# Performance work log

Measured on AMD Instinct MI355X. Metric: run time of the kernel, lower is better.

Reference implementation:

```python
import jax, jax.numpy as jnp
import numpy as np

BITWIDTH = 8
T = 1 << BITWIDTH          # bit-stream length = 2**bitwidth = 256
B = 16                     # independent unary streams
IN1, H1, H2, OUT = 1024, 512, 256, 10


def sobol_rng(bitwidth=BITWIDTH):
    # 1-D unscrambled Sobol sequence (== torch.quasirandom.SobolEngine(1)),
    n = 1 << bitwidth
    i = np.arange(n, dtype=np.uint32)
    g = i ^ (i >> 1)  # Gray code
    x = np.zeros(n, dtype=np.float64)
    for j in range(bitwidth):
        x += ((g >> np.uint32(j)) & np.uint32(1)).astype(np.float64) * 2.0 ** -(j + 1)
    return jnp.asarray(x * 2.0 - 1.0, dtype=jnp.float32)


def _forward(w1, b1, w2, b2, w3, b3, prediction, x):
    rng = sobol_rng()
    f32 = jnp.float32
    Bn = x.shape[1]

    def lin_state(fin, fout):
        # rng_wght_idx rows are all identical in the torch code (the [1, fin]
        # input broadcasts across [fout, fin]), so we keep only [B, fin].
        return (jnp.zeros((Bn, fin), jnp.int32),   # rng_wght_idx
                jnp.zeros((Bn, fin), jnp.int32),   # rng_wght_idx_inv
                jnp.zeros((Bn, fout), f32),        # in_accumulator
                jnp.zeros((Bn, fout), f32))        # out_accumulator

    def ulinear(state, xf, xi, w, bvec, t, offset):
        cum, cum_inv, in_acc, out_acc = state
        # regenerate binary weight matrices by compare against gathered rng
        w_pos = (w[None, :, :] > rng[cum][:, None, :]).astype(f32)      # [B, fout, fin]
        w_neg = (w[None, :, :] <= rng[cum_inv][:, None, :]).astype(f32)  # [B, fout, fin]
        bias_bit = (bvec > rng[t]).astype(f32)                           # [fout]
        y = (jnp.einsum('bi,boi->bo', xf, w_pos)
             + jnp.einsum('bi,boi->bo', 1.0 - xf, w_neg)
             + bias_bit[None, :])
        in_acc = in_acc + y - offset
        out = (in_acc > out_acc).astype(f32)
        out_acc = out_acc + out
        return (cum + xi, cum_inv + (1 - xi), in_acc, out_acc), out

    def ucompare(acc, inp):  # unary ReLU (UnaryCompare)
        sign = (acc < 0).astype(f32)
        out = sign + (1.0 - sign) * inp
        return acc + 2.0 * out - 1.0, out

    def step(carry, xs_t):
        s1, c1, s2, c2, s3 = carry
        xi, t = xs_t
        xf = xi.astype(f32)
        s1, y1 = ulinear(s1, xf, xi, w1, b1, t, (IN1 - 1) / 2)
        c1, a1 = ucompare(c1, y1)
        s2, y2 = ulinear(s2, a1, a1.astype(jnp.int32), w2, b2, t, (H1 - 1) / 2)
        c2, a2 = ucompare(c2, y2)
        s3, y3 = ulinear(s3, a2, a2.astype(jnp.int32), w3, b3, t, (H2 - 1) / 2)
        # ProgressivePrecision is re-created every forward: out_pp = 2*y3 - 1,
        # err = out_pp - prediction, then log_softmax.
        out_t = jax.nn.log_softmax(2.0 * y3 - 1.0 - prediction, axis=1)
        return (s1, c1, s2, c2, s3), out_t

    init = (lin_state(IN1, H1), jnp.zeros((Bn, H1), f32),
            lin_state(H1, H2), jnp.zeros((Bn, H2), f32),
            lin_state(H2, OUT))
    _, outs = jax.lax.scan(step, init, (x, jnp.arange(T)))
    return outs  # [T, B, OUT]


def setup_inputs():
    key = jax.random.key(0)
    ks = jax.random.split(key, 8)
    u = lambda k, s: jax.random.uniform(k, s, jnp.float32, -1.0, 1.0)
    return {
        'w1': u(ks[0], (H1, IN1)), 'b1': u(ks[1], (H1,)),
        'w2': u(ks[2], (H2, H1)), 'b2': u(ks[3], (H2,)),
        'w3': u(ks[4], (OUT, H2)), 'b3': u(ks[5], (OUT,)),
        'prediction': 0.1 * jax.random.normal(ks[6], (B, OUT), jnp.float32),
        'x': jax.random.randint(ks[7], (T, B, IN1), 0, 2, jnp.int32),
    }


def reference(w1, b1, w2, b2, w3, b3, prediction, x):
    return _forward(w1, b1, w2, b2, w3, b3, prediction, x)
```

## Files before the change

### kernel.cpp

```cpp
#include <hip/hip_runtime.h>
#include <stdint.h>

#define TSTEPS 256
#define NB 16
#define NM (TSTEPS*NB)

typedef short s16x2 __attribute__((ext_vector_type(2)));

__device__ __forceinline__ uint32_t perm8(int i) {
  uint32_t g = (uint32_t)(i ^ (i >> 1));
  return __brev(g) >> 24;
}

__device__ __forceinline__ void qstep3s(uint32_t& acc, uint32_t t2, uint32_t a2,
                                        uint32_t e2, uint32_t c15) {
  uint32_t z, z2;
  asm("v_pk_mad_i16 %0, %1, %2, %3" : "=v"(z) : "v"(a2), "s"(t2), "v"(e2));
  asm("v_pk_ashrrev_i16 %0, %1, %2" : "=v"(z2) : "v"(c15), "v"(z));
  asm("v_pk_add_i16 %0, %0, %1" : "+v"(acc) : "v"(z2));
}

__device__ __forceinline__ void qstep3(uint32_t& acc, uint32_t t2, uint32_t a2,
                                       uint32_t e2, uint32_t c15) {
  uint32_t z;
  asm("v_pk_mad_i16 %0, %2, %3, %4\n\t"
      "v_pk_ashrrev_i16 %0, %5, %0\n\t"
      "v_pk_add_i16 %1, %1, %0"
      : "=&v"(z), "+v"(acc)
      : "v"(a2), "v"(t2), "v"(e2), "v"(c15));
}

__device__ __forceinline__ uint32_t pkadd16(uint32_t a, uint32_t b) {
  return __builtin_bit_cast(uint32_t,
        (s16x2)(__builtin_bit_cast(s16x2, a) + __builtin_bit_cast(s16x2, b)));
}

__device__ __forceinline__ void unpackAE(uint32_t v2, uint32_t& a2, uint32_t& e2) {
  s16x2 sv = __builtin_bit_cast(s16x2, v2) >> 15;
  uint32_t su = __builtin_bit_cast(uint32_t, sv);
  uint32_t vand = v2 & 0x01FF01FFu;
  e2 = pkadd16(~vand, su & 0x01FF01FFu);
  a2 = pkadd16(0x00010001u, pkadd16(su, su));
}

__device__ __forceinline__ int rank256(float w) {
  double v = 128.0 * (double)w + 128.0;
  int t = (int)ceil(v);
  if (t < 0) t = 0; if (t > 256) t = 256;
  return t;
}

__global__ __launch_bounds__(256) void k_prepA(
    const float* __restrict__ w1, const float* __restrict__ w2,
    const float* __restrict__ w3, const float* __restrict__ b1,
    const float* __restrict__ b2, const float* __restrict__ b3,
    const int* __restrict__ x,
    uint32_t* __restrict__ T1, uint32_t* __restrict__ T2,
    uint32_t* __restrict__ T3t, uint32_t* __restrict__ bb1,
    uint32_t* __restrict__ bb2, uint32_t* __restrict__ bb3,
    uint16_t* __restrict__ cs)
{
  int bid = blockIdx.x, tid = threadIdx.x;
  if (bid < 1024) {
    int e = bid * 256 + tid;
    T1[e] = (uint32_t)rank256(w1[2 * e]) |
            ((uint32_t)rank256(w1[2 * e + 1]) << 16);
  } else if (bid < 1280) {
    int e = (bid - 1024) * 256 + tid;
    T2[e] = (uint32_t)rank256(w2[2 * e]) |
            ((uint32_t)rank256(w2[2 * e + 1]) << 16);
  } else if (bid < 1285) {
    int e = (bid - 1280) * 256 + tid;
    if (e < 1280) {
      int n = e % 10, kp = e / 10;
      T3t[e] = (uint32_t)rank256(w3[n * 256 + 2 * kp]) |
               ((uint32_t)rank256(w3[n * 256 + 2 * kp + 1]) << 16);
    }
  } else if (bid < 1301) {
    int w = (bid - 1285) * 256 + tid;
    int o = w >> 3, j = w & 7;
    double bv = (double)b1[o] * 128.0 + 128.0;
    uint32_t bits = 0;
    for (int s = 0; s < 32; ++s)
      if (bv > (double)perm8(j * 32 + s)) bits |= 1u << s;
    bb1[w] = bits;
  } else if (bid < 1309) {
    int w = (bid - 1301) * 256 + tid;
    int o = w >> 3, j = w & 7;
    double bv = (double)b2[o] * 128.0 + 128.0;
    uint32_t bits = 0;
    for (int s = 0; s < 32; ++s)
      if (bv > (double)perm8(j * 32 + s)) bits |= 1u << s;
    bb2[w] = bits;
  } else if (bid == 1309) {
    if (tid < 80) {
      int o = tid >> 3, j = tid & 7;
      double bv = (double)b3[o] * 128.0 + 128.0;
      uint32_t bits = 0;
      for (int s = 0; s < 32; ++s)
        if (bv > (double)perm8(j * 32 + s)) bits |= 1u << s;
      bb3[tid] = bits;
    }
  } else {
    int g = (bid - 1310) * 256 + tid;
    int i = g & 1023, b = (g >> 10) & 15, c = g >> 14;
    int s = 0, t0 = c * 32;
    for (int tt = t0; tt < t0 + 32; ++tt)
      s += x[((size_t)tt * NB + b) * 1024 + i];
    cs[(c * NB + b) * 1024 + i] = (uint16_t)s;
  }
}

__global__ __launch_bounds__(256) void k_prep1(const int* __restrict__ x,
                                               const uint16_t* __restrict__ cs,
                                               uint16_t* __restrict__ V1) {
  int g = blockIdx.x * 256 + threadIdx.x;
  int i = g & 1023, b = (g >> 10) & 15, c = g >> 14;
  int cum = 0;
  for (int cc = 0; cc < c; ++cc) cum += cs[(cc * NB + b) * 1024 + i];
  int t0 = c * 32;
  for (int tt = t0; tt < t0 + 32; ++tt) {
    int m = b * 256 + tt;
    int xv = x[((size_t)tt * NB + b) * 1024 + i];
    int idx = xv ? cum : (tt - cum);
    uint32_t p = perm8(idx);
    V1[(size_t)m * 1024 + i] =
        (uint16_t)((xv ? p : (510u - p)) | ((uint32_t)(xv ^ 1) << 15));
    cum += xv;
  }
}

template<int KD, int NT, int NREG, int KC>
__global__ __launch_bounds__(256, 4) void k_gemmv4(
    const uint16_t* __restrict__ V, const uint32_t* __restrict__ T,
    uint8_t* __restrict__ Yp)
{
  const int tid = threadIdx.x;
  const int m = blockIdx.x * 256 + tid;
  const int n0 = blockIdx.y * NREG;
  const int sk = blockIdx.z;
  const int k0 = sk * KC;
  const uint32_t c15 = 0x000F000Fu;
  uint32_t acc[NREG];
  #pragma unroll
  for (int nn = 0; nn < NREG; ++nn) acc[nn] = 0;
  const uint4* vsrc = (const uint4*)(V + (size_t)m * KD + k0);
  const uint32_t* tbase = T + (size_t)n0 * (KD / 2) + (k0 >> 1);
  #pragma unroll 1
  for (int c = 0; c < KC / 8; ++c) {
    uint4 vv = vsrc[c];
    uint32_t a0, e0, a1, e1, a2v, e2v, a3, e3;
    unpackAE(vv.x, a0, e0);
    unpackAE(vv.y, a1, e1);
    unpackAE(vv.z, a2v, e2v);
    unpackAE(vv.w, a3, e3);
    asm volatile("" : "+v"(a0), "+v"(e0), "+v"(a1), "+v"(e1),
                      "+v"(a2v), "+v"(e2v), "+v"(a3), "+v"(e3));
    #pragma unroll
    for (int nn = 0; nn < NREG; ++nn) {
      uint4 tw = *(const uint4*)(tbase + (size_t)nn * (KD / 2) + c * 4);
      qstep3s(acc[nn], tw.x, a0, e0, c15);
      qstep3s(acc[nn], tw.y, a1, e1, c15);
      qstep3s(acc[nn], tw.z, a2v, e2v, c15);
      qstep3s(acc[nn], tw.w, a3, e3, c15);
    }
  }
  uint8_t* outp = Yp + ((size_t)sk * NT + n0) * (size_t)NM + m;
  #pragma unroll
  for (int nn = 0; nn < NREG; ++nn) {
    uint32_t s = acc[nn];
    int cnt = KC + (int)(short)(s & 0xFFFFu) + (int)(short)(s >> 16);
    outp[(size_t)nn * NM] = (uint8_t)cnt;
  }
}

__global__ __launch_bounds__(256) void k_sumY(
    const uint8_t* __restrict__ Yp, uint16_t* __restrict__ Ys,
    int nwords, size_t plane_words, int SK)
{
  int i = blockIdx.x * 256 + threadIdx.x;
  if (i >= nwords) return;
  const uint32_t* p = (const uint32_t*)Yp;
  uint32_t aL = 0, aH = 0;
  for (int s = 0; s < SK; ++s) {
    uint32_t w = p[(size_t)s * plane_words + i];
    aL = pkadd16(aL, w & 0x00FF00FFu);
    aH = pkadd16(aH, (w >> 8) & 0x00FF00FFu);
  }
  uint2 o;
  o.x = (aL & 0xFFFFu) | (aH << 16);
  o.y = (aL >> 16) | (aH & 0xFFFF0000u);
  ((uint2*)Ys)[i] = o;
}

template<int NOUT, int OFF2, int LOGN>
__global__ __launch_bounds__(64) void k_scanv2(
    const uint16_t* __restrict__ Ys, const uint32_t* __restrict__ bb,
    uint16_t* __restrict__ Vn)
{
  int g = blockIdx.x * 64 + threadIdx.x;
  int o = g & (NOUT - 1);
  int b = g >> LOGN;
  const uint16_t* row = Ys + (size_t)o * NM + b * 256;
  int in2 = 0, out2 = 0, c2 = 0, cum = 0;
  uint4 cur = *(const uint4*)row;
  #pragma unroll
  for (int w = 0; w < 8; ++w) {
    uint32_t bwc = bb[o * 8 + w];
    #pragma unroll
    for (int cchunk = 0; cchunk < 4; ++cchunk) {
      int t0 = w * 32 + cchunk * 8;
      uint4 nxt = cur;
      if (t0 < 248) nxt = *(const uint4*)(row + t0 + 8);
      uint32_t cw[4] = {cur.x, cur.y, cur.z, cur.w};
      #pragma unroll
      for (int j = 0; j < 8; ++j) {
        int t = t0 + j;
        int cnt = (int)((cw[j >> 1] >> ((j & 1) * 16)) & 0xFFFFu);
        int bit = (int)((bwc >> (t & 31)) & 1u);
        in2 += 2 * cnt + 2 * bit - OFF2;
        int outb = (in2 > out2) ? 1 : 0;
        out2 += outb << 1;
        int a = (c2 < 0) ? 1 : outb;
        c2 += (a << 2) - 2;
        int idx = a ? cum : (t - cum);
        cum += a;
        uint32_t p = perm8(idx);
        Vn[(size_t)(b * 256 + t) * NOUT + o] =
            (uint16_t)((a ? p : (510u - p)) | ((uint32_t)(a ^ 1) << 15));
      }
      cur = nxt;
    }
  }
}

__global__ __launch_bounds__(256) void k_l3(
    const uint16_t* __restrict__ V3, const uint32_t* __restrict__ T3t,
    uint16_t* __restrict__ y3)
{
  __shared__ uint32_t T3s[128][16];
  __shared__ uint32_t UFs3[16][258];
  int tid = threadIdx.x;
  int m0 = blockIdx.x * 16;
  const uint32_t c15 = 0x000F000Fu;
  for (int j = tid; j < 2048; j += 256) {
    int kp = j >> 4, o2 = j & 15;
    T3s[kp][o2] = (o2 < 10) ? T3t[kp * 10 + o2] : 0u;
  }
  { int row = tid >> 4, part = tid & 15;
    const uint4* src = (const uint4*)(V3 + (size_t)(m0 + row) * 256 + part * 16);
    uint4 pa = src[0], pb = src[1];
    uint32_t w[8] = {pa.x, pa.y, pa.z, pa.w, pb.x, pb.y, pb.z, pb.w};
    uint32_t o[16];
    #pragma unroll
    for (int q = 0; q < 8; ++q) unpackAE(w[q], o[q * 2], o[q * 2 + 1]);
    #pragma unroll
    for (int q4 = 0; q4 < 4; ++q4)
      *(uint4*)&UFs3[row][part * 16 + q4 * 4] =
          make_uint4(o[q4 * 4], o[q4 * 4 + 1], o[q4 * 4 + 2], o[q4 * 4 + 3]);
  }
  __syncthreads();
  int mr = tid >> 4, o = tid & 15;
  uint32_t acc = 0;
  #pragma unroll 4
  for (int kp2 = 0; kp2 < 64; ++kp2) {
    uint4 uf = *(const uint4*)&UFs3[mr][kp2 * 4];
    qstep3(acc, T3s[2 * kp2][o],     uf.x, uf.y, c15);
    qstep3(acc, T3s[2 * kp2 + 1][o], uf.z, uf.w, c15);
  }
  if (o < 10)
    y3[(size_t)(m0 + mr) * 16 + o] =
        (uint16_t)(256 + (short)(acc & 0xFFFFu) + (short)(acc >> 16));
}

__global__ __launch_bounds__(256) void k_scan3sm(
    const uint16_t* __restrict__ y3, const uint32_t* __restrict__ bb3,
    const float* __restrict__ pred, float* __restrict__ out)
{
  __shared__ uint32_t obl[16][16][8];
  __shared__ float prs[160];
  int tid = threadIdx.x;
  if (tid < 160) prs[tid] = pred[tid];
  int b = tid >> 4, o = tid & 15;
  if (o < 10) {
    const uint16_t* row = y3 + (size_t)b * 256 * 16 + o;
    int in2 = 0, out2 = 0;
    #pragma unroll
    for (int w = 0; w < 8; ++w) {
      uint32_t bwc = bb3[o * 8 + w];
      uint32_t bits = 0;
      for (int s = 0; s < 32; ++s) {
        int cnt = row[(w * 32 + s) * 16];
        in2 += 2 * cnt + 2 * (int)((bwc >> s) & 1u) - 255;
        int outb = (in2 > out2) ? 1 : 0;
        out2 += outb << 1;
        bits |= (uint32_t)outb << s;
      }
      obl[b][o][w] = bits;
    }
  }
  __syncthreads();
  for (int r = tid; r < 4096; r += 256) {
    int t = r >> 4, b2 = r & 15;
    float z[10], mx = -3e38f;
    #pragma unroll
    for (int oo = 0; oo < 10; ++oo) {
      int bit = (obl[b2][oo][t >> 5] >> (t & 31)) & 1;
      z[oo] = (bit ? 1.f : -1.f) - prs[b2 * 10 + oo];
      mx = fmaxf(mx, z[oo]);
    }
    float s = 0.f;
    #pragma unroll
    for (int oo = 0; oo < 10; ++oo) s += expf(z[oo] - mx);
    float ls = logf(s);
    float* op = out + (size_t)r * 10;
    #pragma unroll
    for (int oo = 0; oo < 10; ++oo) op[oo] = z[oo] - mx - ls;
  }
}

extern "C" void kernel_launch(void* const* d_in, const int* in_sizes, int n_in,
                              void* d_out, int out_size, void* d_ws, size_t ws_size,
                              hipStream_t stream) {
  (void)in_sizes; (void)n_in; (void)out_size; (void)ws_size;
  const float* w1   = (const float*)d_in[0];
  const float* b1   = (const float*)d_in[1];
  const float* w2   = (const float*)d_in[2];
  const float* b2   = (const float*)d_in[3];
  const float* w3   = (const float*)d_in[4];
  const float* b3   = (const float*)d_in[5];
  const float* pred = (const float*)d_in[6];
  const int*   x    = (const int*)d_in[7];
  float* out = (float*)d_out;
  uint8_t* W = (uint8_t*)d_ws;

  uint32_t* T1   = (uint32_t*)(W + 0);
  uint32_t* T2   = (uint32_t*)(W + 1048576);
  uint32_t* T3t  = (uint32_t*)(W + 1310720);
  uint32_t* bb1  = (uint32_t*)(W + 1318912);
  uint32_t* bb2  = (uint32_t*)(W + 1335296);
  uint32_t* bb3  = (uint32_t*)(W + 1343488);
  uint16_t* chks = (uint16_t*)(W + 1344000);
  uint16_t* V1   = (uint16_t*)(W + 1606144);
  uint16_t* Ys1  = (uint16_t*)(W + 1606144);
  uint16_t* V2   = (uint16_t*)(W + 5800448);
  uint8_t*  Yp1  = (uint8_t*) (W + 9994752);
  uint8_t*  Yp2  = (uint8_t*) (W + 9994752);
  uint16_t* Ys2  = (uint16_t*)(W + 26771968);
  uint16_t* V3   = (uint16_t*)(W + 28869120);
  uint16_t* Y3   = (uint16_t*)(W + 30966272);

  hipLaunchKernelGGL(k_prepA, dim3(1822), dim3(256), 0, stream,
                     w1, w2, w3, b1, b2, b3, x, T1, T2, T3t, bb1, bb2, bb3, chks);
  hipLaunchKernelGGL(k_prep1, dim3(512), dim3(256), 0, stream, x, chks, V1);
  hipLaunchKernelGGL((k_gemmv4<1024, 512, 16, 128>), dim3(16, 32, 8), dim3(256),
                     0, stream, V1, T1, Yp1);
  hipLaunchKernelGGL(k_sumY, dim3(2048), dim3(256), 0, stream,
                     Yp1, Ys1, 512 * NM / 4, (size_t)(512 * NM / 4), 8);
  hipLaunchKernelGGL((k_scanv2<512, 1023, 9>), dim3(128), dim3(64), 0, stream,
                     Ys1, bb1, V2);
  hipLaunchKernelGGL((k_gemmv4<512, 256, 16, 128>), dim3(16, 16, 4), dim3(256),
                     0, stream, V2, T2, Yp2);
  hipLaunchKernelGGL(k_sumY, dim3(1024), dim3(256), 0, stream,
                     Yp2, Ys2, 256 * NM / 4, (size_t)(256 * NM / 4), 4);
  hipLaunchKernelGGL((k_scanv2<256, 511, 8>), dim3(64), dim3(64), 0, stream,
                     Ys2, bb2, V3);
  hipLaunchKernelGGL(k_l3, dim3(256), dim3(256), 0, stream, V3, T3t, Y3);
  hipLaunchKernelGGL(k_scan3sm, dim3(1), dim3(256), 0, stream, Y3, bb3, pred, out);
}
```

Measured before the change: 228.3 us.

## Use SAD-based byte accumulation in GEMM and fold split-K reduction into scan

The packed-int16 inner step (mad, arithmetic shift, add) becomes a mad followed by a byte permute that collects the sign bytes and a v_sad_u8 accumulation. This shortens the per-weight instruction chain. The split-K partials are now written as 16-bit values and summed directly inside the serial scan kernel, so the separate k_sumY reduction kernel is removed. The scan recurrence is rescaled by a constant so it can work on raw SAD sums. Layer 1 also moves to a larger split-K chunk (KC=256, NREG=32, 4 splits), which cuts partial traffic but raises register pressure and means the latency-bound scan now does four loads per step.

Measured after the change: 277.8 us. 1.22x slower.

```diff
diff --git a/kernel.cpp b/kernel.cpp
--- a/kernel.cpp
+++ b/kernel.cpp
@@ -12,12 +12,17 @@
   return __brev(g) >> 24;
 }
 
-__device__ __forceinline__ void qstep3s(uint32_t& acc, uint32_t t2, uint32_t a2,
-                                        uint32_t e2, uint32_t c15) {
-  uint32_t z, z2;
-  asm("v_pk_mad_i16 %0, %1, %2, %3" : "=v"(z) : "v"(a2), "s"(t2), "v"(e2));
-  asm("v_pk_ashrrev_i16 %0, %1, %2" : "=v"(z2) : "v"(c15), "v"(z));
-  asm("v_pk_add_i16 %0, %0, %1" : "+v"(acc) : "v"(z2));
+__device__ __forceinline__ void qmad(uint32_t& z, uint32_t a, uint32_t t_s,
+                                     uint32_t e) {
+  asm("v_pk_mad_i16 %0, %1, %2, %3" : "=v"(z) : "v"(a), "s"(t_s), "v"(e));
+}
+__device__ __forceinline__ uint32_t qperm(uint32_t x, uint32_t y, uint32_t sel) {
+  uint32_t d;
+  asm("v_perm_b32 %0, %1, %2, %3" : "=v"(d) : "v"(x), "v"(y), "v"(sel));
+  return d;
+}
+__device__ __forceinline__ void qsad(uint32_t& acc, uint32_t p) {
+  asm("v_sad_u8 %0, %1, 0, %0" : "+v"(acc) : "v"(p));
 }
 
 __device__ __forceinline__ void qstep3(uint32_t& acc, uint32_t t2, uint32_t a2,
@@ -49,6 +54,10 @@
   if (t < 0) t = 0; if (t > 256) t = 256;
   return t;
 }
+
+#define SUMLOHI(A,B,C,D, LO, HI) \
+  LO = (A & 0xFFFFu) + (B & 0xFFFFu) + (C & 0xFFFFu) + (D & 0xFFFFu); \
+  HI = (A >> 16) + (B >> 16) + (C >> 16) + (D >> 16);
 
 __global__ __launch_bounds__(256) void k_prepA(
     const float* __restrict__ w1, const float* __restrict__ w2,
@@ -131,16 +140,16 @@
 }
 
 template<int KD, int NT, int NREG, int KC>
-__global__ __launch_bounds__(256, 4) void k_gemmv4(
+__global__ __launch_bounds__(256, 4) void k_gemmv5(
     const uint16_t* __restrict__ V, const uint32_t* __restrict__ T,
-    uint8_t* __restrict__ Yp)
+    uint16_t* __restrict__ Yp)
 {
   const int tid = threadIdx.x;
   const int m = blockIdx.x * 256 + tid;
   const int n0 = blockIdx.y * NREG;
   const int sk = blockIdx.z;
   const int k0 = sk * KC;
-  const uint32_t c15 = 0x000F000Fu;
+  uint32_t sel = 0x07050301u;
   uint32_t acc[NREG];
   #pragma unroll
   for (int nn = 0; nn < NREG; ++nn) acc[nn] = 0;
@@ -159,77 +168,71 @@
     #pragma unroll
     for (int nn = 0; nn < NREG; ++nn) {
       uint4 tw = *(const uint4*)(tbase + (size_t)nn * (KD / 2) + c * 4);
-      qstep3s(acc[nn], tw.x, a0, e0, c15);
-      qstep3s(acc[nn], tw.y, a1, e1, c15);
-      qstep3s(acc[nn], tw.z, a2v, e2v, c15);
-      qstep3s(acc[nn], tw.w, a3, e3, c15);
-    }
-  }
-  uint8_t* outp = Yp + ((size_t)sk * NT + n0) * (size_t)NM + m;
+      uint32_t z0, z1, z2, z3;
+      qmad(z0, a0, tw.x, e0);
+      qmad(z1, a1, tw.y, e1);
+      qmad(z2, a2v, tw.z, e2v);
+      qmad(z3, a3, tw.w, e3);
+      qsad(acc[nn], qperm(z0, z1, sel));
+      qsad(acc[nn], qperm(z2, z3, sel));
+    }
+  }
+  uint16_t* outp = Yp + ((size_t)sk * NT + n0) * (size_t)NM + m;
   #pragma unroll
-  for (int nn = 0; nn < NREG; ++nn) {
-    uint32_t s = acc[nn];
-    int cnt = KC + (int)(short)(s & 0xFFFFu) + (int)(short)(s >> 16);
-    outp[(size_t)nn * NM] = (uint8_t)cnt;
-  }
-}
-
-__global__ __launch_bounds__(256) void k_sumY(
-    const uint8_t* __restrict__ Yp, uint16_t* __restrict__ Ys,
-    int nwords, size_t plane_words, int SK)
-{
-  int i = blockIdx.x * 256 + threadIdx.x;
-  if (i >= nwords) return;
-  const uint32_t* p = (const uint32_t*)Yp;
-  uint32_t aL = 0, aH = 0;
-  for (int s = 0; s < SK; ++s) {
-    uint32_t w = p[(size_t)s * plane_words + i];
-    aL = pkadd16(aL, w & 0x00FF00FFu);
-    aH = pkadd16(aH, (w >> 8) & 0x00FF00FFu);
-  }
-  uint2 o;
-  o.x = (aL & 0xFFFFu) | (aH << 16);
-  o.y = (aL >> 16) | (aH & 0xFFFF0000u);
-  ((uint2*)Ys)[i] = o;
-}
-
-template<int NOUT, int OFF2, int LOGN>
-__global__ __launch_bounds__(64) void k_scanv2(
-    const uint16_t* __restrict__ Ys, const uint32_t* __restrict__ bb,
+  for (int nn = 0; nn < NREG; ++nn)
+    outp[(size_t)nn * NM] = (uint16_t)acc[nn];
+}
+
+template<int NOUT, int KD, int OFF2, int LOGN>
+__global__ __launch_bounds__(64) void k_scanv3(
+    const uint16_t* __restrict__ Yp, const uint32_t* __restrict__ bb,
     uint16_t* __restrict__ Vn)
 {
+  const size_t PS = (size_t)NOUT * NM;
   int g = blockIdx.x * 64 + threadIdx.x;
   int o = g & (NOUT - 1);
   int b = g >> LOGN;
-  const uint16_t* row = Ys + (size_t)o * NM + b * 256;
-  int in2 = 0, out2 = 0, c2 = 0, cum = 0;
-  uint4 cur = *(const uint4*)row;
+  const uint16_t* row = Yp + (size_t)o * NM + b * 256;
+  const int C = 255 * (2 * KD - OFF2);
+  int inA = 0, outA = 0, cA = 0, cum = 0;
+  uint4 c0 = *(const uint4*)(row);
+  uint4 c1 = *(const uint4*)(row + PS);
+  uint4 c2 = *(const uint4*)(row + 2 * PS);
+  uint4 c3 = *(const uint4*)(row + 3 * PS);
   #pragma unroll
   for (int w = 0; w < 8; ++w) {
     uint32_t bwc = bb[o * 8 + w];
     #pragma unroll
     for (int cchunk = 0; cchunk < 4; ++cchunk) {
       int t0 = w * 32 + cchunk * 8;
-      uint4 nxt = cur;
-      if (t0 < 248) nxt = *(const uint4*)(row + t0 + 8);
-      uint32_t cw[4] = {cur.x, cur.y, cur.z, cur.w};
+      uint4 n0v = c0, n1v = c1, n2v = c2, n3v = c3;
+      if (t0 < 248) {
+        n0v = *(const uint4*)(row + t0 + 8);
+        n1v = *(const uint4*)(row + PS + t0 + 8);
+        n2v = *(const uint4*)(row + 2 * PS + t0 + 8);
+        n3v = *(const uint4*)(row + 3 * PS + t0 + 8);
+      }
+      uint32_t s[8];
+      SUMLOHI(c0.x, c1.x, c2.x, c3.x, s[0], s[1]);
+      SUMLOHI(c0.y, c1.y, c2.y, c3.y, s[2], s[3]);
+      SUMLOHI(c0.z, c1.z, c2.z, c3.z, s[4], s[5]);
+      SUMLOHI(c0.w, c1.w, c2.w, c3.w, s[6], s[7]);
       #pragma unroll
       for (int j = 0; j < 8; ++j) {
         int t = t0 + j;
-        int cnt = (int)((cw[j >> 1] >> ((j & 1) * 16)) & 0xFFFFu);
         int bit = (int)((bwc >> (t & 31)) & 1u);
-        in2 += 2 * cnt + 2 * bit - OFF2;
-        int outb = (in2 > out2) ? 1 : 0;
-        out2 += outb << 1;
-        int a = (c2 < 0) ? 1 : outb;
-        c2 += (a << 2) - 2;
+        inA += C + 510 * bit - 2 * (int)s[j];
+        int outb = (inA > outA) ? 1 : 0;
+        outA += 510 * outb;
+        int a = (cA < 0) ? 1 : outb;
+        cA += 1020 * a - 510;
         int idx = a ? cum : (t - cum);
         cum += a;
         uint32_t p = perm8(idx);
         Vn[(size_t)(b * 256 + t) * NOUT + o] =
             (uint16_t)((a ? p : (510u - p)) | ((uint32_t)(a ^ 1) << 15));
       }
-      cur = nxt;
+      c0 = n0v; c1 = n1v; c2 = n2v; c3 = n3v;
     }
   }
 }
@@ -342,29 +345,23 @@
   uint32_t* bb3  = (uint32_t*)(W + 1343488);
   uint16_t* chks = (uint16_t*)(W + 1344000);
   uint16_t* V1   = (uint16_t*)(W + 1606144);
-  uint16_t* Ys1  = (uint16_t*)(W + 1606144);
   uint16_t* V2   = (uint16_t*)(W + 5800448);
-  uint8_t*  Yp1  = (uint8_t*) (W + 9994752);
-  uint8_t*  Yp2  = (uint8_t*) (W + 9994752);
-  uint16_t* Ys2  = (uint16_t*)(W + 26771968);
+  uint16_t* Yp1  = (uint16_t*)(W + 9994752);
+  uint16_t* Yp2  = (uint16_t*)(W + 9994752);
   uint16_t* V3   = (uint16_t*)(W + 28869120);
   uint16_t* Y3   = (uint16_t*)(W + 30966272);
 
   hipLaunchKernelGGL(k_prepA, dim3(1822), dim3(256), 0, stream,
                      w1, w2, w3, b1, b2, b3, x, T1, T2, T3t, bb1, bb2, bb3, chks);
   hipLaunchKernelGGL(k_prep1, dim3(512), dim3(256), 0, stream, x, chks, V1);
-  hipLaunchKernelGGL((k_gemmv4<1024, 512, 16, 128>), dim3(16, 32, 8), dim3(256),
+  hipLaunchKernelGGL((k_gemmv5<1024, 512, 32, 256>), dim3(16, 16, 4), dim3(256),
                      0, stream, V1, T1, Yp1);
-  hipLaunchKernelGGL(k_sumY, dim3(2048), dim3(256), 0, stream,
-                     Yp1, Ys1, 512 * NM / 4, (size_t)(512 * NM / 4), 8);
-  hipLaunchKernelGGL((k_scanv2<512, 1023, 9>), dim3(128), dim3(64), 0, stream,
-                     Ys1, bb1, V2);
-  hipLaunchKernelGGL((k_gemmv4<512, 256, 16, 128>), dim3(16, 16, 4), dim3(256),
+  hipLaunchKernelGGL((k_scanv3<512, 1024, 1023, 9>), dim3(128), dim3(64), 0,
+                     stream, Yp1, bb1, V2);
+  hipLaunchKernelGGL((k_gemmv5<512, 256, 16, 128>), dim3(16, 16, 4), dim3(256),
                      0, stream, V2, T2, Yp2);
-  hipLaunchKernelGGL(k_sumY, dim3(1024), dim3(256), 0, stream,
-                     Yp2, Ys2, 256 * NM / 4, (size_t)(256 * NM / 4), 4);
-  hipLaunchKernelGGL((k_scanv2<256, 511, 8>), dim3(64), dim3(64), 0, stream,
-                     Ys2, bb2, V3);
+  hipLaunchKernelGGL((k_scanv3<256, 512, 511, 8>), dim3(64), dim3(64), 0,
+                     stream, Yp2, bb2, V3);
   hipLaunchKernelGGL(k_l3, dim3(256), dim3(256), 0, stream, V3, T3t, Y3);
   hipLaunchKernelGGL(k_scan3sm, dim3(1), dim3(256), 0, stream, Y3, bb3, pred, out);
 }
```
